# Kernel tuning notes

Measured on AMD Instinct MI355X. Metric: run time of the kernel, lower is better.

Reference implementation:

```python
import jax, jax.numpy as jnp
import numpy as np

N = 8192   # instances in bag
L = 384    # feature dim (dino_bloom_small -> self.L = 384)
D = 128    # attention hidden dim (self.D)
C = 5      # class_count


def setup_inputs() -> dict:
    key = jax.random.key(0)
    ks = jax.random.split(key, 9)
    s = 0.05
    return {
        "x": jax.random.normal(ks[0], (N, L), dtype=jnp.float32),
        # attention_multi_column: Linear(L,D) -> Tanh -> Linear(D,C)
        "aW1": jax.random.normal(ks[1], (L, D), dtype=jnp.float32) * s,
        "ab1": jax.random.normal(ks[2], (D,), dtype=jnp.float32) * s,
        "aW2": jax.random.normal(ks[3], (D, C), dtype=jnp.float32) * s,
        "ab2": jax.random.normal(ks[4], (C,), dtype=jnp.float32) * s,
        # per-class classifiers: Linear(L,64) -> ReLU -> Linear(64,1), batched over C
        "cW1": jax.random.normal(ks[5], (C, L, 64), dtype=jnp.float32) * s,
        "cb1": jax.random.normal(ks[6], (C, 64), dtype=jnp.float32) * s,
        "cW2": jax.random.normal(ks[7], (C, 64), dtype=jnp.float32) * s,
        "cb2": jax.random.normal(ks[8], (C,), dtype=jnp.float32) * s,
    }


def _pairwise_euclidean(ft):
    # ||a-b|| via Gram expansion; avoids the O(N^2*L) broadcast intermediate
    sq = jnp.sum(ft * ft, axis=1)                      # [N]
    d2 = sq[:, None] + sq[None, :] - 2.0 * (ft @ ft.T)  # [N,N]
    d2 = jnp.maximum(d2, 0.0)
    # safe sqrt (zero on diagonal, matches torch.norm subgradient convention)
    return jnp.where(d2 > 0.0, jnp.sqrt(jnp.where(d2 > 0.0, d2, 1.0)), 0.0)


def reference(x, aW1, ab1, aW2, ab2, cW1, cb1, cW2, cb2):
    ft = x  # encoder is identity for dino_bloom_small
    dist = _pairwise_euclidean(ft)                      # [N,N]
    # multicolumn attention: logits per class, softmax over instances
    att = jnp.tanh(ft @ aW1 + ab1) @ aW2 + ab2          # [N,C]
    att_sm = jax.nn.softmax(att, axis=0)                # softmax over N per class
    bag = att_sm.T @ ft                                 # [C,L] bag features per class
    # per-class classifier heads, batched over class dim
    h = jax.nn.relu(jnp.einsum('cl,clh->ch', bag, cW1) + cb1)  # [C,64]
    pred = jnp.sum(h * cW2, axis=1) + cb2               # [C]
    return pred[None, :], dist
```

## Files before the change

### kernel.cpp

```cpp
#include <hip/hip_runtime.h>
#include <cstdint>
#include <cstddef>

#define N_INST 8192
#define L_DIM  384
#define D_DIM  128
#define C_CLS  5

typedef __bf16 bf16x8 __attribute__((ext_vector_type(8)));
typedef float  f32x4  __attribute__((ext_vector_type(4)));
typedef float  f32x4u __attribute__((ext_vector_type(4), aligned(4)));

typedef __attribute__((address_space(1))) void gvoid_t;
typedef __attribute__((address_space(3))) void lvoid_t;

__device__ __forceinline__ unsigned short f2bf(float f) {
  unsigned u = __float_as_uint(f);
  unsigned r = (u + 0x7FFFu + ((u >> 16) & 1u)) >> 16;
  return (unsigned short)r;
}
__device__ __forceinline__ float bf2f(unsigned short b) {
  return __uint_as_float(((unsigned)b) << 16);
}

__device__ __forceinline__ void gload_lds16(const void* g, void* lds) {
  __builtin_amdgcn_global_load_lds(
      (gvoid_t*)(uintptr_t)g,
      (lvoid_t*)(uint32_t)(uintptr_t)lds,
      16, 0, 0);
}

__global__ __launch_bounds__(256) void prep_x_kernel(
    const float* __restrict__ x, unsigned short* __restrict__ xbf,
    float* __restrict__ sq) {
  int w = threadIdx.x >> 6, lane = threadIdx.x & 63;
  int row = blockIdx.x * 4 + w;
  const float* xr = x + (size_t)row * L_DIM;
  unsigned short* br = xbf + (size_t)row * L_DIM;
  float s = 0.f;
#pragma unroll
  for (int k = 0; k < 6; ++k) {
    float v = xr[lane + 64 * k];
    unsigned short b = f2bf(v);
    br[lane + 64 * k] = b;
    float vb = bf2f(b);
    s = fmaf(vb, vb, s);
  }
#pragma unroll
  for (int off = 32; off; off >>= 1) s += __shfl_down(s, off, 64);
  if (lane == 0) sq[row] = s;
}

__global__ __launch_bounds__(256) void prep_w_kernel(
    const float* __restrict__ aW1, unsigned short* __restrict__ w1t) {
  int idx = blockIdx.x * 256 + threadIdx.x;
  int d = idx / L_DIM, l = idx - d * L_DIM;
  w1t[idx] = f2bf(aW1[(size_t)l * D_DIM + d]);
}

__global__ __launch_bounds__(256, 2) void attn_gemm_kernel(
    const unsigned short* __restrict__ amat,
    const unsigned short* __restrict__ bmat,
    const float* __restrict__ bias,
    float* __restrict__ out) {
  __shared__ alignas(16) unsigned short As[128][64];
  __shared__ alignas(16) unsigned short Bs[128][64];

  int tid = threadIdx.x;
  int w = tid >> 6, lane = tid & 63;
  int wr = w >> 1, wc = w & 1;
  int i0 = blockIdx.x * 128;

  const unsigned short* asrc = amat + (size_t)i0 * L_DIM;
  const unsigned short* bsrc = bmat;

  f32x4 acc[4][4];
#pragma unroll
  for (int m = 0; m < 4; ++m)
#pragma unroll
    for (int n = 0; n < 4; ++n) acc[m][n] = (f32x4){0.f, 0.f, 0.f, 0.f};

  int lrow = lane & 15, lkb = lane >> 4;

  for (int kc = 0; kc < 6; ++kc) {
    int k0 = kc * 64;
#pragma unroll
    for (int c = 0; c < 4; ++c) {
      int rb = c * 32 + w * 8;
      gload_lds16(asrc + (size_t)(rb + (lane >> 3)) * L_DIM + k0 + (lane & 7) * 8,
                  &As[rb][0]);
      gload_lds16(bsrc + (size_t)(rb + (lane >> 3)) * L_DIM + k0 + (lane & 7) * 8,
                  &Bs[rb][0]);
    }
    __syncthreads();
#pragma unroll
    for (int kk = 0; kk < 64; kk += 32) {
      bf16x8 af[4], bfr[4];
#pragma unroll
      for (int m = 0; m < 4; ++m)
        af[m] = *(const bf16x8*)&As[wr * 64 + m * 16 + lrow][kk + lkb * 8];
#pragma unroll
      for (int n = 0; n < 4; ++n)
        bfr[n] = *(const bf16x8*)&Bs[wc * 64 + n * 16 + lrow][kk + lkb * 8];
#pragma unroll
      for (int m = 0; m < 4; ++m)
#pragma unroll
        for (int n = 0; n < 4; ++n)
          acc[m][n] = __builtin_amdgcn_mfma_f32_16x16x32_bf16(
              bfr[n], af[m], acc[m][n], 0, 0, 0);
    }
    __syncthreads();
  }
#pragma unroll
  for (int m = 0; m < 4; ++m) {
    int gi = i0 + wr * 64 + m * 16 + lrow;
    float* orow = out + (size_t)gi * D_DIM;
#pragma unroll
    for (int n = 0; n < 4; ++n) {
      int d0 = wc * 64 + n * 16 + lkb * 4;
      f32x4 bv = *(const f32x4*)&bias[d0];
      f32x4 o;
#pragma unroll
      for (int r = 0; r < 4; ++r) o[r] = tanhf(acc[m][n][r] + bv[r]);
      *(f32x4*)&orow[d0] = o;
    }
  }
}

__global__ __launch_bounds__(256) void head_kernel(
    const unsigned short* __restrict__ xbf, const float* __restrict__ sqv,
    float* __restrict__ F) {
  int w = threadIdx.x >> 6, lane = threadIdx.x & 63;
  int i = blockIdx.x * 4 + w;
  float a0 = 0.f, a1 = 0.f, a2 = 0.f;
  if (lane < 48) {
    const unsigned short* xi = xbf + (size_t)i * L_DIM + lane * 8;
    const unsigned short* x0 = xbf + lane * 8;
    const unsigned short* x1 = xbf + L_DIM + lane * 8;
    const unsigned short* x2 = xbf + 2 * L_DIM + lane * 8;
#pragma unroll
    for (int e = 0; e < 8; ++e) {
      float v = bf2f(xi[e]);
      a0 = fmaf(v, bf2f(x0[e]), a0);
      a1 = fmaf(v, bf2f(x1[e]), a1);
      a2 = fmaf(v, bf2f(x2[e]), a2);
    }
  }
#pragma unroll
  for (int off = 32; off; off >>= 1) {
    a0 += __shfl_down(a0, off, 64);
    a1 += __shfl_down(a1, off, 64);
    a2 += __shfl_down(a2, off, 64);
  }
  if (lane == 0) {
    float si = sqv[i];
    float dots[3] = {a0, a1, a2};
#pragma unroll
    for (int j = 0; j < 3; ++j) {
      float d2 = si + sqv[j] - 2.f * dots[j];
      float dv = (d2 > 0.f) ? sqrtf(d2) : 0.f;
      if (i == j) dv = 0.f;
      F[5 + (size_t)i * N_INST + j] = dv;
    }
  }
}

__global__ __launch_bounds__(256, 2) void dist_kernel(
    const unsigned short* __restrict__ xbf, const float* __restrict__ sqv,
    float* __restrict__ F) {
  __shared__ alignas(16) unsigned short As[128][64];
  __shared__ alignas(16) unsigned short Bs[128][64];

  int tid = threadIdx.x;
  int w = tid >> 6, lane = tid & 63;
  int wr = w >> 1, wc = w & 1;

  int b = blockIdx.x;
  int ti = b >> 6, tj = b & 63;
  int i0 = ti * 128, j0 = tj * 128;

  const unsigned short* asrc = xbf + (size_t)i0 * L_DIM;
  const unsigned short* bsrc = xbf + (size_t)(j0 + 3) * L_DIM;

  f32x4 acc[4][4];
#pragma unroll
  for (int m = 0; m < 4; ++m)
#pragma unroll
    for (int n = 0; n < 4; ++n) acc[m][n] = (f32x4){0.f, 0.f, 0.f, 0.f};

  int lrow = lane & 15, lkb = lane >> 4;
  int schunk = ((lane & 7) ^ (lane >> 3)) * 8;
  int swz = (lane & 7) << 3;

  for (int kc = 0; kc < 6; ++kc) {
    int k0 = kc * 64;
#pragma unroll
    for (int c = 0; c < 4; ++c) {
      int rb = c * 32 + w * 8;
      gload_lds16(asrc + (size_t)(rb + (lane >> 3)) * L_DIM + k0 + schunk,
                  &As[rb][0]);
      gload_lds16(bsrc + (size_t)(rb + (lane >> 3)) * L_DIM + k0 + schunk,
                  &Bs[rb][0]);
    }
    __syncthreads();
#pragma unroll
    for (int kk = 0; kk < 64; kk += 32) {
      bf16x8 af[4], bfr[4];
#pragma unroll
      for (int m = 0; m < 4; ++m)
        af[m] = *(const bf16x8*)&As[wr * 64 + m * 16 + lrow][(kk + lkb * 8) ^ swz];
#pragma unroll
      for (int n = 0; n < 4; ++n)
        bfr[n] = *(const bf16x8*)&Bs[wc * 64 + n * 16 + lrow][(kk + lkb * 8) ^ swz];
#pragma unroll
      for (int m = 0; m < 4; ++m)
#pragma unroll
        for (int n = 0; n < 4; ++n)
          acc[m][n] = __builtin_amdgcn_mfma_f32_16x16x32_bf16(
              bfr[n], af[m], acc[m][n], 0, 0, 0);
    }
    __syncthreads();
  }

#pragma unroll
  for (int m = 0; m < 4; ++m) {
    int gi = i0 + wr * 64 + m * 16 + lrow;
    float si = sqv[gi];
    float* orow = F + 5 + (size_t)gi * N_INST;
#pragma unroll
    for (int n = 0; n < 4; ++n) {
      int gjb = j0 + 3 + wc * 64 + n * 16 + lkb * 4;
      f32x4u sj = *(const f32x4u*)&sqv[gjb];
      f32x4 o;
#pragma unroll
      for (int r = 0; r < 4; ++r) {
        float d2 = si + sj[r] - 2.f * acc[m][n][r];
        float dv = (d2 > 0.f) ? sqrtf(d2) : 0.f;
        if (gi == gjb + r) dv = 0.f;
        o[r] = dv;
      }
      if (gjb + 3 < N_INST) {
        *(f32x4*)&orow[gjb] = o;
      } else {
        orow[N_INST - 1] = o[0];
      }
    }
  }
}

__global__ __launch_bounds__(256) void attc_kernel(
    const float* __restrict__ h, const float* __restrict__ aW2,
    const float* __restrict__ ab2, float* __restrict__ exp_att,
    float* __restrict__ colsum) {
  __shared__ float csum[C_CLS];
  if (threadIdx.x < C_CLS) csum[threadIdx.x] = 0.f;
  __syncthreads();
  int i = blockIdx.x * 256 + threadIdx.x;
  float a[C_CLS];
#pragma unroll
  for (int c = 0; c < C_CLS; ++c) a[c] = ab2[c];
  const float* hr = h + (size_t)i * D_DIM;
  for (int d = 0; d < D_DIM; ++d) {
    float hv = hr[d];
#pragma unroll
    for (int c = 0; c < C_CLS; ++c) a[c] = fmaf(hv, aW2[d * C_CLS + c], a[c]);
  }
#pragma unroll
  for (int c = 0; c < C_CLS; ++c) {
    float e = expf(a[c]);
    exp_att[(size_t)i * C_CLS + c] = e;
    atomicAdd(&csum[c], e);
  }
  __syncthreads();
  if (threadIdx.x < C_CLS) atomicAdd(&colsum[threadIdx.x], csum[threadIdx.x]);
}

__global__ __launch_bounds__(256) void bag_kernel(
    const float* __restrict__ x, const float* __restrict__ exp_att,
    float* __restrict__ bagU) {
  int t = threadIdx.x;
  int rbase = blockIdx.x * 32;
  float acc0[C_CLS] = {0, 0, 0, 0, 0}, acc1[C_CLS] = {0, 0, 0, 0, 0};
  int l0 = t, l1 = t + 256;
  for (int i = rbase; i < rbase + 32; ++i) {
    const float* xr = x + (size_t)i * L_DIM;
    float e[C_CLS];
#pragma unroll
    for (int c = 0; c < C_CLS; ++c) e[c] = exp_att[(size_t)i * C_CLS + c];
    float x0 = xr[l0];
#pragma unroll
    for (int c = 0; c < C_CLS; ++c) acc0[c] = fmaf(e[c], x0, acc0[c]);
    if (t < 128) {
      float x1 = xr[l1];
#pragma unroll
      for (int c = 0; c < C_CLS; ++c) acc1[c] = fmaf(e[c], x1, acc1[c]);
    }
  }
#pragma unroll
  for (int c = 0; c < C_CLS; ++c) atomicAdd(&bagU[c * L_DIM + l0], acc0[c]);
  if (t < 128)
#pragma unroll
    for (int c = 0; c < C_CLS; ++c) atomicAdd(&bagU[c * L_DIM + l1], acc1[c]);
}

__global__ __launch_bounds__(256) void final_kernel(
    const float* __restrict__ bagU, const float* __restrict__ colsum,
    const float* __restrict__ cW1, const float* __restrict__ cb1,
    const float* __restrict__ cW2, const float* __restrict__ cb2,
    float* __restrict__ out) {
  __shared__ float bag_s[C_CLS * L_DIM];
  __shared__ float h_s[C_CLS * 64];
  int t = threadIdx.x;
  for (int idx = t; idx < C_CLS * L_DIM; idx += 256) {
    int c = idx / L_DIM;
    bag_s[idx] = bagU[idx] / colsum[c];
  }
  __syncthreads();
  for (int idx = t; idx < C_CLS * 64; idx += 256) {
    int c = idx >> 6, hh = idx & 63;
    float acc = cb1[idx];
    for (int l = 0; l < L_DIM; ++l)
      acc = fmaf(bag_s[c * L_DIM + l], cW1[(size_t)(c * L_DIM + l) * 64 + hh], acc);
    h_s[idx] = fmaxf(acc, 0.f) * cW2[idx];
  }
  __syncthreads();
  if (t < C_CLS) {
    float p = cb2[t];
    for (int hh = 0; hh < 64; ++hh) p += h_s[t * 64 + hh];
    out[t] = p;
  }
}

extern "C" void kernel_launch(void* const* d_in, const int* in_sizes, int n_in,
                              void* d_out, int out_size, void* d_ws,
                              size_t ws_size, hipStream_t stream) {
  const float* x   = (const float*)d_in[0];
  const float* aW1 = (const float*)d_in[1];
  const float* ab1 = (const float*)d_in[2];
  const float* aW2 = (const float*)d_in[3];
  const float* ab2 = (const float*)d_in[4];
  const float* cW1 = (const float*)d_in[5];
  const float* cb1 = (const float*)d_in[6];
  const float* cW2 = (const float*)d_in[7];
  const float* cb2 = (const float*)d_in[8];
  float* outp = (float*)d_out;

  char* ws = (char*)d_ws;
  unsigned short* xbf = (unsigned short*)(ws);
  unsigned short* w1t = (unsigned short*)(ws + 6291456);
  float* sq           = (float*)(ws + 6389760);
  float* h_tanh       = (float*)(ws + 6422528);
  float* exp_att      = (float*)(ws + 10616832);
  float* colsum       = (float*)(ws + 10780672);
  float* bagU         = (float*)(ws + 10780736);

  hipMemsetAsync(ws + 10780672, 0, 64 + C_CLS * L_DIM * 4, stream);

  prep_x_kernel<<<2048, 256, 0, stream>>>(x, xbf, sq);
  prep_w_kernel<<<192, 256, 0, stream>>>(aW1, w1t);
  attn_gemm_kernel<<<64, 256, 0, stream>>>(xbf, w1t, ab1, h_tanh);
  attc_kernel<<<32, 256, 0, stream>>>(h_tanh, aW2, ab2, exp_att, colsum);
  bag_kernel<<<256, 256, 0, stream>>>(x, exp_att, bagU);
  final_kernel<<<1, 256, 0, stream>>>(bagU, colsum, cW1, cb1, cW2, cb2, outp);
  head_kernel<<<2048, 256, 0, stream>>>(xbf, sq, outp);
  dist_kernel<<<4096, 256, 0, stream>>>(xbf, sq, outp);
}
```

Baseline: 191.1 us.

## Exploit distance symmetry with triangular tiles and fuse attention logits into GEMM

```diff
diff --git a/kernel.cpp b/kernel.cpp
--- a/kernel.cpp
+++ b/kernel.cpp
@@ -62,14 +62,23 @@
     const unsigned short* __restrict__ amat,
     const unsigned short* __restrict__ bmat,
     const float* __restrict__ bias,
-    float* __restrict__ out) {
+    const float* __restrict__ aW2,
+    const float* __restrict__ ab2,
+    float* __restrict__ exp_att,
+    float* __restrict__ colsum) {
   __shared__ alignas(16) unsigned short As[128][64];
   __shared__ alignas(16) unsigned short Bs[128][64];
+  __shared__ float aW2_l[D_DIM * C_CLS];
+  __shared__ float part[128][8][C_CLS];
+  __shared__ float cs_l[C_CLS];
 
   int tid = threadIdx.x;
   int w = tid >> 6, lane = tid & 63;
   int wr = w >> 1, wc = w & 1;
   int i0 = blockIdx.x * 128;
+
+  for (int idx = tid; idx < D_DIM * C_CLS; idx += 256) aW2_l[idx] = aW2[idx];
+  if (tid < C_CLS) cs_l[tid] = 0.f;
 
   const unsigned short* asrc = amat + (size_t)i0 * L_DIM;
   const unsigned short* bsrc = bmat;
@@ -111,20 +120,46 @@
     }
     __syncthreads();
   }
+
+  int q = wc * 4 + lkb;
 #pragma unroll
   for (int m = 0; m < 4; ++m) {
-    int gi = i0 + wr * 64 + m * 16 + lrow;
-    float* orow = out + (size_t)gi * D_DIM;
+    int row_l = wr * 64 + m * 16 + lrow;
+    float p[C_CLS] = {0.f, 0.f, 0.f, 0.f, 0.f};
 #pragma unroll
     for (int n = 0; n < 4; ++n) {
       int d0 = wc * 64 + n * 16 + lkb * 4;
-      f32x4 bv = *(const f32x4*)&bias[d0];
-      f32x4 o;
-#pragma unroll
-      for (int r = 0; r < 4; ++r) o[r] = tanhf(acc[m][n][r] + bv[r]);
-      *(f32x4*)&orow[d0] = o;
-    }
-  }
+#pragma unroll
+      for (int r = 0; r < 4; ++r) {
+        float v = tanhf(acc[m][n][r] + bias[d0 + r]);
+        const float* wrow = &aW2_l[(d0 + r) * C_CLS];
+#pragma unroll
+        for (int c = 0; c < C_CLS; ++c) p[c] = fmaf(v, wrow[c], p[c]);
+      }
+    }
+#pragma unroll
+    for (int c = 0; c < C_CLS; ++c) part[row_l][q][c] = p[c];
+  }
+  __syncthreads();
+
+  if (tid < 128) {
+    int gi = i0 + tid;
+    float a[C_CLS];
+#pragma unroll
+    for (int c = 0; c < C_CLS; ++c) a[c] = ab2[c];
+#pragma unroll
+    for (int qq = 0; qq < 8; ++qq)
+#pragma unroll
+      for (int c = 0; c < C_CLS; ++c) a[c] += part[tid][qq][c];
+#pragma unroll
+    for (int c = 0; c < C_CLS; ++c) {
+      float e = expf(a[c]);
+      exp_att[(size_t)gi * C_CLS + c] = e;
+      atomicAdd(&cs_l[c], e);
+    }
+  }
+  __syncthreads();
+  if (tid < C_CLS) atomicAdd(&colsum[tid], cs_l[tid]);
 }
 
 __global__ __launch_bounds__(256) void head_kernel(
@@ -176,11 +211,14 @@
   int wr = w >> 1, wc = w & 1;
 
   int b = blockIdx.x;
-  int ti = b >> 6, tj = b & 63;
+  int ti = (int)((129.0 - sqrt(129.0 * 129.0 - 8.0 * (double)b)) * 0.5);
+  while ((ti + 1) * (129 - (ti + 1)) / 2 <= b) ++ti;
+  while (ti * (129 - ti) / 2 > b) --ti;
+  int tj = ti + (b - ti * (129 - ti) / 2);
   int i0 = ti * 128, j0 = tj * 128;
 
   const unsigned short* asrc = xbf + (size_t)i0 * L_DIM;
-  const unsigned short* bsrc = xbf + (size_t)(j0 + 3) * L_DIM;
+  const unsigned short* bsrc = xbf + (size_t)j0 * L_DIM;
 
   f32x4 acc[4][4];
 #pragma unroll
@@ -222,6 +260,7 @@
     __syncthreads();
   }
 
+  bool mirror = (ti != tj);
 #pragma unroll
   for (int m = 0; m < 4; ++m) {
     int gi = i0 + wr * 64 + m * 16 + lrow;
@@ -229,9 +268,9 @@
     float* orow = F + 5 + (size_t)gi * N_INST;
 #pragma unroll
     for (int n = 0; n < 4; ++n) {
-      int gjb = j0 + 3 + wc * 64 + n * 16 + lkb * 4;
-      f32x4u sj = *(const f32x4u*)&sqv[gjb];
-      f32x4 o;
+      int gjb = j0 + wc * 64 + n * 16 + lkb * 4;
+      f32x4 sj = *(const f32x4*)&sqv[gjb];
+      f32x4u o;
 #pragma unroll
       for (int r = 0; r < 4; ++r) {
         float d2 = si + sj[r] - 2.f * acc[m][n][r];
@@ -239,40 +278,14 @@
         if (gi == gjb + r) dv = 0.f;
         o[r] = dv;
       }
-      if (gjb + 3 < N_INST) {
-        *(f32x4*)&orow[gjb] = o;
-      } else {
-        orow[N_INST - 1] = o[0];
+      *(f32x4u*)&orow[gjb] = o;
+      if (mirror) {
+#pragma unroll
+        for (int r = 0; r < 4; ++r)
+          F[5 + (size_t)(gjb + r) * N_INST + gi] = o[r];
       }
     }
   }
-}
-
-__global__ __launch_bounds__(256) void attc_kernel(
-    const float* __restrict__ h, const float* __restrict__ aW2,
-    const float* __restrict__ ab2, float* __restrict__ exp_att,
-    float* __restrict__ colsum) {
-  __shared__ float csum[C_CLS];
-  if (threadIdx.x < C_CLS) csum[threadIdx.x] = 0.f;
-  __syncthreads();
-  int i = blockIdx.x * 256 + threadIdx.x;
-  float a[C_CLS];
-#pragma unroll
-  for (int c = 0; c < C_CLS; ++c) a[c] = ab2[c];
-  const float* hr = h + (size_t)i * D_DIM;
-  for (int d = 0; d < D_DIM; ++d) {
-    float hv = hr[d];
-#pragma unroll
-    for (int c = 0; c < C_CLS; ++c) a[c] = fmaf(hv, aW2[d * C_CLS + c], a[c]);
-  }
-#pragma unroll
-  for (int c = 0; c < C_CLS; ++c) {
-    float e = expf(a[c]);
-    exp_att[(size_t)i * C_CLS + c] = e;
-    atomicAdd(&csum[c], e);
-  }
-  __syncthreads();
-  if (threadIdx.x < C_CLS) atomicAdd(&colsum[threadIdx.x], csum[threadIdx.x]);
 }
 
 __global__ __launch_bounds__(256) void bag_kernel(
@@ -349,19 +362,18 @@
   unsigned short* xbf = (unsigned short*)(ws);
   unsigned short* w1t = (unsigned short*)(ws + 6291456);
   float* sq           = (float*)(ws + 6389760);
-  float* h_tanh       = (float*)(ws + 6422528);
-  float* exp_att      = (float*)(ws + 10616832);
-  float* colsum       = (float*)(ws + 10780672);
-  float* bagU         = (float*)(ws + 10780736);
-
-  hipMemsetAsync(ws + 10780672, 0, 64 + C_CLS * L_DIM * 4, stream);
+  float* exp_att      = (float*)(ws + 6422528);
+  float* colsum       = (float*)(ws + 6586368);
+  float* bagU         = (float*)(ws + 6586432);
+
+  hipMemsetAsync(ws + 6586368, 0, 64 + C_CLS * L_DIM * 4, stream);
 
   prep_x_kernel<<<2048, 256, 0, stream>>>(x, xbf, sq);
   prep_w_kernel<<<192, 256, 0, stream>>>(aW1, w1t);
-  attn_gemm_kernel<<<64, 256, 0, stream>>>(xbf, w1t, ab1, h_tanh);
-  attc_kernel<<<32, 256, 0, stream>>>(h_tanh, aW2, ab2, exp_att, colsum);
+  attn_gemm_kernel<<<64, 256, 0, stream>>>(xbf, w1t, ab1, aW2, ab2, exp_att,
+                                           colsum);
   bag_kernel<<<256, 256, 0, stream>>>(x, exp_att, bagU);
   final_kernel<<<1, 256, 0, stream>>>(bagU, colsum, cW1, cb1, cW2, cb2, outp);
   head_kernel<<<2048, 256, 0, stream>>>(xbf, sq, outp);
-  dist_kernel<<<4096, 256, 0, stream>>>(xbf, sq, outp);
-}
+  dist_kernel<<<2080, 256, 0, stream>>>(xbf, sq, outp);
+}
```

Result: slower. 210.2 us (+10.0%).
